# Optimization experiments

Hardware: AMD Instinct MI355X
Metric: run time of the kernel (lower is better)

The kernel has to match this reference:

```python
import jax, jax.numpy as jnp
import numpy as np

B, S, D_MODEL, D_K = 4, 4096, 1024, 64


def setup_inputs() -> dict:
    key = jax.random.key(0)
    kx, kq, kk, kv = jax.random.split(key, 4)
    x = jax.random.normal(kx, (B, S, D_MODEL), dtype=jnp.float32)
    # Linear(in, out) stores weight as (out, in); y = x @ W^T, no bias
    Wq = jax.random.normal(kq, (D_K, D_MODEL), dtype=jnp.float32) * (D_MODEL ** -0.5)
    Wk = jax.random.normal(kk, (D_K, D_MODEL), dtype=jnp.float32) * (D_MODEL ** -0.5)
    Wv = jax.random.normal(kv, (D_MODEL, D_MODEL), dtype=jnp.float32) * (D_MODEL ** -0.5)
    return {"x": x, "Wq": Wq, "Wk": Wk, "Wv": Wv}


def reference(x, Wq, Wk, Wv):
    # single-head scaled dot-product attention
    q = jnp.einsum('bsd,kd->bsk', x, Wq)   # [B,S,d_k]
    k = jnp.einsum('bsd,kd->bsk', x, Wk)   # [B,S,d_k]
    v = jnp.einsum('bsd,md->bsm', x, Wv)   # [B,S,d_model]
    scale = 1.0 / jnp.sqrt(jnp.asarray(q.shape[-1], q.dtype))
    scores = jnp.einsum('bqk,bsk->bqs', q, k) * scale  # [B,S,S]
    probs = jax.nn.softmax(scores, axis=-1)
    return jnp.einsum('bqs,bsm->bqm', probs, v)        # [B,S,d_model]
```

## Files before the change

kernel.cpp:

```cpp
#include <hip/hip_runtime.h>


#define DEV static __device__ __forceinline__

typedef __attribute__((ext_vector_type(8))) short bf16x8;
typedef __attribute__((ext_vector_type(4))) float f32x4;
typedef __attribute__((ext_vector_type(4))) unsigned short u16x4;
typedef __attribute__((ext_vector_type(8))) unsigned short u16x8;
typedef __attribute__((address_space(1))) void as1_void;
typedef __attribute__((address_space(3))) void as3_void;

DEV unsigned short f2bf(float f) {
  union { float f; unsigned u; } v; v.f = f;
  return (unsigned short)((v.u + 0x7FFFu + ((v.u >> 16) & 1u)) >> 16);
}

DEV unsigned pk_bf16(float a, float b) {
  union { float f; unsigned u; } va, vb;
  va.f = a; vb.f = b;
  return __builtin_amdgcn_perm(vb.u + 0x8000u, va.u + 0x8000u, 0x07060302u);
}

DEV void gload16(const void* g, void* l) {
  __builtin_amdgcn_global_load_lds((as1_void*)g, (as3_void*)l, 16, 0, 0);
}

DEV int swz(int row, int cb) { return (row << 7) + (cb ^ ((row & 7) << 4)); }

DEV void lgkm_barrier() {
  asm volatile("s_waitcnt lgkmcnt(0)" ::: "memory");
  __builtin_amdgcn_sched_barrier(0);
  __builtin_amdgcn_s_barrier();
  __builtin_amdgcn_sched_barrier(0);
}

__global__ __launch_bounds__(256) void cast_all_k(
    const float* __restrict__ x, const float* __restrict__ wq,
    const float* __restrict__ wk, const float* __restrict__ wv,
    unsigned short* __restrict__ xb, unsigned short* __restrict__ wcat, float sq) {
  const int stride = gridDim.x * blockDim.x;
  for (int i = blockIdx.x * blockDim.x + threadIdx.x; i < 2244608; i += stride) {
    const float* src; unsigned short* dst; float scale; int j;
    if (i < 2097152)      { src = x;  dst = xb;            scale = 1.f; j = i; }
    else if (i < 2105344) { src = wq; dst = wcat;          scale = sq;  j = i - 2097152; }
    else if (i < 2113536) { src = wk; dst = wcat + 65536;  scale = 1.f; j = i - 2105344; }
    else                  { src = wv; dst = wcat + 131072; scale = 1.f; j = i - 2113536; }
    const float4* p = (const float4*)src + (size_t)j * 2;
    float4 a = p[0], b = p[1];
    u16x8 r;
    r[0] = f2bf(a.x * scale); r[1] = f2bf(a.y * scale);
    r[2] = f2bf(a.z * scale); r[3] = f2bf(a.w * scale);
    r[4] = f2bf(b.x * scale); r[5] = f2bf(b.y * scale);
    r[6] = f2bf(b.z * scale); r[7] = f2bf(b.w * scale);
    *(u16x8*)(dst + (size_t)j * 8) = r;
  }
}

__global__ __launch_bounds__(256, 2) void gemm_qkv_k(
    const unsigned short* __restrict__ xb, const unsigned short* __restrict__ wcat,
    unsigned short* __restrict__ qk, unsigned short* __restrict__ vT) {
  __shared__ __align__(16) unsigned char smem[65536];
  unsigned char* sA = smem;
  unsigned char* sB = smem + 32768;
  const int tid = threadIdx.x;
  const int w = tid >> 6, lane = tid & 63, lo = lane & 15, hi = lane >> 4;
  const int wr = w >> 1, wc = w & 1;
  const int bn = blockIdx.x, m0 = blockIdx.y * 128, n0 = bn * 128;
  const char* aBase = (const char*)xb + (size_t)m0 * 2048;
  const char* bBase = (const char*)wcat + (size_t)n0 * 2048;

  const int soff = ((w * 4) << 10) + (lane << 4);
  f32x4 acc[4][4];
  const f32x4 z = {0.f, 0.f, 0.f, 0.f};
#pragma unroll
  for (int mi = 0; mi < 4; ++mi)
#pragma unroll
    for (int ni = 0; ni < 4; ++ni) acc[mi][ni] = z;

#pragma unroll
  for (int r2 = 0; r2 < 4; ++r2) {
    const int off = soff + (r2 << 10);
    const int row = off >> 7;
    const int cbs = (off & 127) ^ ((row & 7) << 4);
    gload16(aBase + (size_t)row * 2048 + cbs, sA + ((w * 4 + r2) << 10));
    gload16(bBase + (size_t)row * 2048 + cbs, sB + ((w * 4 + r2) << 10));
  }
  __syncthreads();

  int cur = 0;
  for (int k0 = 0; k0 < 1024; k0 += 64) {
    if (k0 + 64 < 1024) {
      const int nb = (cur ^ 1) * 16384;
#pragma unroll
      for (int r2 = 0; r2 < 4; ++r2) {
        const int off = soff + (r2 << 10);
        const int row = off >> 7;
        const int cbs = (off & 127) ^ ((row & 7) << 4);
        gload16(aBase + (size_t)row * 2048 + (k0 + 64) * 2 + cbs, sA + nb + ((w * 4 + r2) << 10));
        gload16(bBase + (size_t)row * 2048 + (k0 + 64) * 2 + cbs, sB + nb + ((w * 4 + r2) << 10));
      }
    }
    const int cb0 = cur * 16384;
#pragma unroll
    for (int kk = 0; kk < 2; ++kk) {
      const int cb = kk * 64 + hi * 16;
      bf16x8 af[4], bfv[4];
#pragma unroll
      for (int mi = 0; mi < 4; ++mi)
        af[mi] = *(const bf16x8*)(sA + cb0 + swz(wr * 64 + mi * 16 + lo, cb));
#pragma unroll
      for (int ni = 0; ni < 4; ++ni)
        bfv[ni] = *(const bf16x8*)(sB + cb0 + swz(wc * 64 + ni * 16 + lo, cb));
#pragma unroll
      for (int mi = 0; mi < 4; ++mi)
#pragma unroll
        for (int ni = 0; ni < 4; ++ni)
          acc[mi][ni] = __builtin_amdgcn_mfma_f32_16x16x32_bf16(af[mi], bfv[ni], acc[mi][ni], 0, 0, 0);
    }
    __syncthreads();
    cur ^= 1;
  }

  if (bn == 0) {
#pragma unroll
    for (int mi = 0; mi < 4; ++mi) {
      const int row = m0 + wr * 64 + mi * 16 + hi * 4;
#pragma unroll
      for (int ni = 0; ni < 4; ++ni) {
        const int col = wc * 64 + ni * 16 + lo;
#pragma unroll
        for (int r = 0; r < 4; ++r)
          qk[(size_t)(row + r) * 128 + col] = f2bf(acc[mi][ni][r]);
      }
    }
  } else {
#pragma unroll
    for (int mi = 0; mi < 4; ++mi) {
      const int grow = m0 + wr * 64 + mi * 16 + hi * 4;
      const int b = grow >> 12, s = grow & 4095;
#pragma unroll
      for (int ni = 0; ni < 4; ++ni) {
        const int vcol = (n0 - 128) + wc * 64 + ni * 16 + lo;
        u16x4 pk;
#pragma unroll
        for (int r = 0; r < 4; ++r) pk[r] = f2bf(acc[mi][ni][r]);
        *(u16x4*)(vT + (size_t)(b * 1024 + vcol) * 4096 + s) = pk;
      }
    }
  }
}

__global__ __launch_bounds__(512, 4) void pv_k(
    const unsigned short* __restrict__ qk, const unsigned short* __restrict__ vT,
    float* __restrict__ out) {
  __shared__ __align__(16) unsigned char smem[57344];
  unsigned char* sK = smem;
  unsigned char* sV = smem + 8192;
  unsigned char* sP = smem + 40960;
  const int tid = threadIdx.x;
  const int w = tid >> 6, lane = tid & 63, lo = lane & 15, hi = lane >> 4;
  const int wr = w >> 2, wc = w & 3;
  const int ck = blockIdx.x, qt = blockIdx.y, b = blockIdx.z;
  const char* qkB = (const char*)qk;
  const char* vTB = (const char*)vT;
  const size_t qrow0 = (size_t)(b * 4096 + qt * 128);
  const f32x4 z = {0.f, 0.f, 0.f, 0.f};

  const int q = w * 16 + lo;
  bf16x8 qf[2];
#pragma unroll
  for (int kk = 0; kk < 2; ++kk)
    qf[kk] = *(const bf16x8*)(qkB + (qrow0 + q) * 256 + kk * 64 + hi * 16);
  float lsum = 0.f;

  const int kc = w * 64 + lane;
  const int kRow = kc >> 3;
  const int kCbs = ((kc & 7) << 4) ^ ((kRow & 7) << 4);
  const char* kSrc = qkB + (size_t)(b * 4096 + kRow) * 256 + 128 + kCbs;

  const int g = lane & 3, dr = (lane >> 2) & 1, qq = lane >> 3;
  const int rr = (qq & 3) + ((qq >> 2) << 3) + (dr << 2);
  const int vRow0 = w * 16 + rr, vRow1 = vRow0 + 128;
  const char* vSrc0 = vTB + (size_t)(b * 1024 + ck * 256 + vRow0) * 8192 + g * 16;
  const char* vSrc1 = vTB + (size_t)(b * 1024 + ck * 256 + vRow1) * 8192 + g * 16;
  unsigned char* vDst0 = sV + vRow0 * 128;
  unsigned char* vDst1 = sV + vRow1 * 128;
  const int vX = g << 4, vR = (vRow0 & 7) << 4;

  const int qx7 = (q & 7) << 4;
  const int aP0 = (q << 7) + ((((hi >> 1) + 0) << 4) ^ qx7) + ((hi & 1) << 3);
  const int aP1 = (q << 7) + ((((hi >> 1) + 2) << 4) ^ qx7) + ((hi & 1) << 3);

  f32x4 acc[4][4];
#pragma unroll
  for (int mi = 0; mi < 4; ++mi)
#pragma unroll
    for (int ni = 0; ni < 4; ++ni) acc[mi][ni] = z;

  {
    float4 v0 = *(const float4*)(vSrc0);
    float4 v1 = *(const float4*)(vSrc1);
    if (w < 4) gload16(kSrc, sK + (w << 10));
    *(float4*)(vDst0 + (vX ^ vR)) = v0;
    *(float4*)(vDst1 + (vX ^ vR)) = v1;
  }
  __syncthreads();

  int cur = 0;
  for (int t = 0; t < 128; ++t) {
    float4 nv0, nv1;
    if (t < 127) {
      nv0 = *(const float4*)(vSrc0 + (size_t)(t + 1) * 64);
      nv1 = *(const float4*)(vSrc1 + (size_t)(t + 1) * 64);
      if (w < 4) gload16(kSrc + (size_t)(t + 1) * 8192, sK + (cur ^ 1) * 4096 + (w << 10));
    }
    f32x4 sv0 = z, sv1 = z;
#pragma unroll
    for (int kk = 0; kk < 2; ++kk) {
      bf16x8 kf0 = *(const bf16x8*)(sK + cur * 4096 + swz(lo, kk * 64 + hi * 16));
      bf16x8 kf1 = *(const bf16x8*)(sK + cur * 4096 + swz(16 + lo, kk * 64 + hi * 16));
      sv0 = __builtin_amdgcn_mfma_f32_16x16x32_bf16(kf0, qf[kk], sv0, 0, 0, 0);
      sv1 = __builtin_amdgcn_mfma_f32_16x16x32_bf16(kf1, qf[kk], sv1, 0, 0, 0);
    }
    {
      const float p0 = __builtin_amdgcn_exp2f(sv0[0]);
      const float p1 = __builtin_amdgcn_exp2f(sv0[1]);
      const float p2 = __builtin_amdgcn_exp2f(sv0[2]);
      const float p3 = __builtin_amdgcn_exp2f(sv0[3]);
      const float p4 = __builtin_amdgcn_exp2f(sv1[0]);
      const float p5 = __builtin_amdgcn_exp2f(sv1[1]);
      const float p6 = __builtin_amdgcn_exp2f(sv1[2]);
      const float p7 = __builtin_amdgcn_exp2f(sv1[3]);
      lsum += ((p0 + p1) + (p2 + p3)) + ((p4 + p5) + (p6 + p7));
      uint2 d0, d1;
      d0.x = pk_bf16(p0, p1); d0.y = pk_bf16(p2, p3);
      d1.x = pk_bf16(p4, p5); d1.y = pk_bf16(p6, p7);
      *(uint2*)(sP + aP0) = d0;
      *(uint2*)(sP + aP1) = d1;
    }
    lgkm_barrier();
    if (t < 127) {
      *(float4*)(vDst0 + ((((cur ^ 1) << 6) + vX) ^ vR)) = nv0;
      *(float4*)(vDst1 + ((((cur ^ 1) << 6) + vX) ^ vR)) = nv1;
    }
    __builtin_amdgcn_s_setprio(1);
    bf16x8 pa[4];
#pragma unroll
    for (int mi = 0; mi < 4; ++mi)
      pa[mi] = *(const bf16x8*)(sP + swz(wr * 64 + mi * 16 + lo, hi * 16));
#pragma unroll
    for (int ni = 0; ni < 4; ++ni) {
      bf16x8 vf = *(const bf16x8*)(sV + swz(wc * 64 + ni * 16 + lo, (cur << 6) + hi * 16));
#pragma unroll
      for (int mi = 0; mi < 4; ++mi)
        acc[mi][ni] = __builtin_amdgcn_mfma_f32_16x16x32_bf16(pa[mi], vf, acc[mi][ni], 0, 0, 0);
    }
    __builtin_amdgcn_s_setprio(0);
    __syncthreads();
    cur ^= 1;
  }

  lsum += __shfl_xor(lsum, 16, 64);
  lsum += __shfl_xor(lsum, 32, 64);
  float* lLds = (float*)smem;
  if (hi == 0) lLds[q] = lsum;
  __syncthreads();

#pragma unroll
  for (int mi = 0; mi < 4; ++mi)
#pragma unroll
    for (int r = 0; r < 4; ++r) {
      const int rloc = wr * 64 + mi * 16 + hi * 4 + r;
      const int grow = (int)qrow0 + rloc;
      const float linv = 1.0f / lLds[rloc];
#pragma unroll
      for (int ni = 0; ni < 4; ++ni) {
        const int col = ck * 256 + wc * 64 + ni * 16 + lo;
        out[(size_t)grow * 1024 + col] = acc[mi][ni][r] * linv;
      }
    }
}

extern "C" void kernel_launch(void* const* d_in, const int* in_sizes, int n_in,
                              void* d_out, int out_size, void* d_ws, size_t ws_size,
                              hipStream_t stream) {
  const float* x  = (const float*)d_in[0];
  const float* Wq = (const float*)d_in[1];
  const float* Wk = (const float*)d_in[2];
  const float* Wv = (const float*)d_in[3];

  char* ws = (char*)d_ws;
  unsigned short* xb    = (unsigned short*)(ws);
  unsigned short* wcat  = (unsigned short*)(ws + 33554432);
  unsigned short* qk    = (unsigned short*)(ws + 35913728);
  unsigned short* vT    = (unsigned short*)(ws + 40108032);

  const float SCALE_Q = 0.125f * 1.4426950408889634f;

  cast_all_k<<<2048, 256, 0, stream>>>(x, Wq, Wk, Wv, xb, wcat, SCALE_Q);
  gemm_qkv_k<<<dim3(9, 128), 256, 0, stream>>>(xb, wcat, qk, vT);
  pv_k<<<dim3(4, 32, 4), 512, 0, stream>>>(qk, vT, (float*)d_out);
}
```

Baseline: 249.3 us.

## Double the key tile per iteration and load V via direct global-to-LDS copies

The PV kernel now processes 64 keys per iteration instead of 32, halving loop trips and barriers. V tiles move from register-staged loads into single-buffered LDS loaded with global_load_lds, issued after the end-of-iteration barrier. K loads are also issued by all waves, and a vmcnt-based wait replaces the old lgkm-only barrier. LDS grows to 64KB, which may limit occupancy, and the single-buffered V load sits on the critical path after each barrier.

```diff
diff --git a/kernel.cpp b/kernel.cpp
--- a/kernel.cpp
+++ b/kernel.cpp
@@ -26,13 +26,6 @@
 }
 
 DEV int swz(int row, int cb) { return (row << 7) + (cb ^ ((row & 7) << 4)); }
-
-DEV void lgkm_barrier() {
-  asm volatile("s_waitcnt lgkmcnt(0)" ::: "memory");
-  __builtin_amdgcn_sched_barrier(0);
-  __builtin_amdgcn_s_barrier();
-  __builtin_amdgcn_sched_barrier(0);
-}
 
 __global__ __launch_bounds__(256) void cast_all_k(
     const float* __restrict__ x, const float* __restrict__ wq,
@@ -153,10 +146,10 @@
 __global__ __launch_bounds__(512, 4) void pv_k(
     const unsigned short* __restrict__ qk, const unsigned short* __restrict__ vT,
     float* __restrict__ out) {
-  __shared__ __align__(16) unsigned char smem[57344];
+  __shared__ __align__(16) unsigned char smem[65536];
   unsigned char* sK = smem;
-  unsigned char* sV = smem + 8192;
-  unsigned char* sP = smem + 40960;
+  unsigned char* sV = smem + 16384;
+  unsigned char* sP = smem + 49152;
   const int tid = threadIdx.x;
   const int w = tid >> 6, lane = tid & 63, lo = lane & 15, hi = lane >> 4;
   const int wr = w >> 2, wc = w & 3;
@@ -174,22 +167,23 @@
   float lsum = 0.f;
 
   const int kc = w * 64 + lane;
-  const int kRow = kc >> 3;
-  const int kCbs = ((kc & 7) << 4) ^ ((kRow & 7) << 4);
-  const char* kSrc = qkB + (size_t)(b * 4096 + kRow) * 256 + 128 + kCbs;
-
-  const int g = lane & 3, dr = (lane >> 2) & 1, qq = lane >> 3;
-  const int rr = (qq & 3) + ((qq >> 2) << 3) + (dr << 2);
-  const int vRow0 = w * 16 + rr, vRow1 = vRow0 + 128;
-  const char* vSrc0 = vTB + (size_t)(b * 1024 + ck * 256 + vRow0) * 8192 + g * 16;
-  const char* vSrc1 = vTB + (size_t)(b * 1024 + ck * 256 + vRow1) * 8192 + g * 16;
-  unsigned char* vDst0 = sV + vRow0 * 128;
-  unsigned char* vDst1 = sV + vRow1 * 128;
-  const int vX = g << 4, vR = (vRow0 & 7) << 4;
+  const int kRow = kc >> 3, kG = kc & 7;
+  const char* kSrc = qkB + (size_t)(b * 4096 + kRow) * 256 + 128 + ((kG ^ (kRow & 7)) << 4);
+  unsigned char* kDst = sK + (kc << 4);
+
+  const char* vSrcJ[4];
+#pragma unroll
+  for (int j = 0; j < 4; ++j) {
+    const int c = tid + j * 512;
+    const int row = c >> 3, g = c & 7;
+    vSrcJ[j] = vTB + (size_t)(b * 1024 + ck * 256 + row) * 8192 + ((g ^ (row & 7)) << 4);
+  }
 
   const int qx7 = (q & 7) << 4;
-  const int aP0 = (q << 7) + ((((hi >> 1) + 0) << 4) ^ qx7) + ((hi & 1) << 3);
-  const int aP1 = (q << 7) + ((((hi >> 1) + 2) << 4) ^ qx7) + ((hi & 1) << 3);
+  const int aP0 = (q << 7) + (((0 + (hi >> 1)) << 4) ^ qx7) + ((hi & 1) << 3);
+  const int aP1 = (q << 7) + (((2 + (hi >> 1)) << 4) ^ qx7) + ((hi & 1) << 3);
+  const int aP2 = (q << 7) + (((4 + (hi >> 1)) << 4) ^ qx7) + ((hi & 1) << 3);
+  const int aP3 = (q << 7) + (((6 + (hi >> 1)) << 4) ^ qx7) + ((hi & 1) << 3);
 
   f32x4 acc[4][4];
 #pragma unroll
@@ -197,66 +191,79 @@
 #pragma unroll
     for (int ni = 0; ni < 4; ++ni) acc[mi][ni] = z;
 
-  {
-    float4 v0 = *(const float4*)(vSrc0);
-    float4 v1 = *(const float4*)(vSrc1);
-    if (w < 4) gload16(kSrc, sK + (w << 10));
-    *(float4*)(vDst0 + (vX ^ vR)) = v0;
-    *(float4*)(vDst1 + (vX ^ vR)) = v1;
-  }
+#pragma unroll
+  for (int j = 0; j < 4; ++j) gload16(vSrcJ[j], sV + ((tid + j * 512) << 4));
+  gload16(kSrc, kDst);
   __syncthreads();
 
   int cur = 0;
-  for (int t = 0; t < 128; ++t) {
-    float4 nv0, nv1;
-    if (t < 127) {
-      nv0 = *(const float4*)(vSrc0 + (size_t)(t + 1) * 64);
-      nv1 = *(const float4*)(vSrc1 + (size_t)(t + 1) * 64);
-      if (w < 4) gload16(kSrc + (size_t)(t + 1) * 8192, sK + (cur ^ 1) * 4096 + (w << 10));
-    }
-    f32x4 sv0 = z, sv1 = z;
+  for (int t = 0; t < 64; ++t) {
+    gload16(kSrc + (size_t)((t + 1) & 63) * 16384, kDst + (cur ^ 1) * 8192);
+    f32x4 sv[4];
+    sv[0] = z; sv[1] = z; sv[2] = z; sv[3] = z;
 #pragma unroll
     for (int kk = 0; kk < 2; ++kk) {
-      bf16x8 kf0 = *(const bf16x8*)(sK + cur * 4096 + swz(lo, kk * 64 + hi * 16));
-      bf16x8 kf1 = *(const bf16x8*)(sK + cur * 4096 + swz(16 + lo, kk * 64 + hi * 16));
-      sv0 = __builtin_amdgcn_mfma_f32_16x16x32_bf16(kf0, qf[kk], sv0, 0, 0, 0);
-      sv1 = __builtin_amdgcn_mfma_f32_16x16x32_bf16(kf1, qf[kk], sv1, 0, 0, 0);
+#pragma unroll
+      for (int n = 0; n < 4; ++n) {
+        bf16x8 kf = *(const bf16x8*)(sK + cur * 8192 + swz(n * 16 + lo, kk * 64 + hi * 16));
+        sv[n] = __builtin_amdgcn_mfma_f32_16x16x32_bf16(kf, qf[kk], sv[n], 0, 0, 0);
+      }
     }
     {
-      const float p0 = __builtin_amdgcn_exp2f(sv0[0]);
-      const float p1 = __builtin_amdgcn_exp2f(sv0[1]);
-      const float p2 = __builtin_amdgcn_exp2f(sv0[2]);
-      const float p3 = __builtin_amdgcn_exp2f(sv0[3]);
-      const float p4 = __builtin_amdgcn_exp2f(sv1[0]);
-      const float p5 = __builtin_amdgcn_exp2f(sv1[1]);
-      const float p6 = __builtin_amdgcn_exp2f(sv1[2]);
-      const float p7 = __builtin_amdgcn_exp2f(sv1[3]);
-      lsum += ((p0 + p1) + (p2 + p3)) + ((p4 + p5) + (p6 + p7));
-      uint2 d0, d1;
-      d0.x = pk_bf16(p0, p1); d0.y = pk_bf16(p2, p3);
-      d1.x = pk_bf16(p4, p5); d1.y = pk_bf16(p6, p7);
+      const float p0 = __builtin_amdgcn_exp2f(sv[0][0]);
+      const float p1 = __builtin_amdgcn_exp2f(sv[0][1]);
+      const float p2 = __builtin_amdgcn_exp2f(sv[0][2]);
+      const float p3 = __builtin_amdgcn_exp2f(sv[0][3]);
+      const float p4 = __builtin_amdgcn_exp2f(sv[1][0]);
+      const float p5 = __builtin_amdgcn_exp2f(sv[1][1]);
+      const float p6 = __builtin_amdgcn_exp2f(sv[1][2]);
+      const float p7 = __builtin_amdgcn_exp2f(sv[1][3]);
+      const float p8 = __builtin_amdgcn_exp2f(sv[2][0]);
+      const float p9 = __builtin_amdgcn_exp2f(sv[2][1]);
+      const float pa_ = __builtin_amdgcn_exp2f(sv[2][2]);
+      const float pb_ = __builtin_amdgcn_exp2f(sv[2][3]);
+      const float pc_ = __builtin_amdgcn_exp2f(sv[3][0]);
+      const float pd_ = __builtin_amdgcn_exp2f(sv[3][1]);
+      const float pe_ = __builtin_amdgcn_exp2f(sv[3][2]);
+      const float pf_ = __builtin_amdgcn_exp2f(sv[3][3]);
+      lsum += (((p0 + p1) + (p2 + p3)) + ((p4 + p5) + (p6 + p7))) +
+              (((p8 + p9) + (pa_ + pb_)) + ((pc_ + pd_) + (pe_ + pf_)));
+      uint2 d0, d1, d2, d3;
+      d0.x = pk_bf16(p0, p1);  d0.y = pk_bf16(p2, p3);
+      d1.x = pk_bf16(p4, p5);  d1.y = pk_bf16(p6, p7);
+      d2.x = pk_bf16(p8, p9);  d2.y = pk_bf16(pa_, pb_);
+      d3.x = pk_bf16(pc_, pd_); d3.y = pk_bf16(pe_, pf_);
       *(uint2*)(sP + aP0) = d0;
       *(uint2*)(sP + aP1) = d1;
-    }
-    lgkm_barrier();
-    if (t < 127) {
-      *(float4*)(vDst0 + ((((cur ^ 1) << 6) + vX) ^ vR)) = nv0;
-      *(float4*)(vDst1 + ((((cur ^ 1) << 6) + vX) ^ vR)) = nv1;
-    }
+      *(uint2*)(sP + aP2) = d2;
+      *(uint2*)(sP + aP3) = d3;
+    }
+    asm volatile("s_waitcnt vmcnt(1) lgkmcnt(0)" ::: "memory");
+    __builtin_amdgcn_sched_barrier(0);
+    __builtin_amdgcn_s_barrier();
+    __builtin_amdgcn_sched_barrier(0);
     __builtin_amdgcn_s_setprio(1);
-    bf16x8 pa[4];
-#pragma unroll
-    for (int mi = 0; mi < 4; ++mi)
-      pa[mi] = *(const bf16x8*)(sP + swz(wr * 64 + mi * 16 + lo, hi * 16));
-#pragma unroll
-    for (int ni = 0; ni < 4; ++ni) {
-      bf16x8 vf = *(const bf16x8*)(sV + swz(wc * 64 + ni * 16 + lo, (cur << 6) + hi * 16));
+#pragma unroll
+    for (int kk = 0; kk < 2; ++kk) {
+      bf16x8 pa[4];
 #pragma unroll
       for (int mi = 0; mi < 4; ++mi)
-        acc[mi][ni] = __builtin_amdgcn_mfma_f32_16x16x32_bf16(pa[mi], vf, acc[mi][ni], 0, 0, 0);
+        pa[mi] = *(const bf16x8*)(sP + swz(wr * 64 + mi * 16 + lo, kk * 64 + hi * 16));
+#pragma unroll
+      for (int ni = 0; ni < 4; ++ni) {
+        bf16x8 vf = *(const bf16x8*)(sV + swz(wc * 64 + ni * 16 + lo, kk * 64 + hi * 16));
+#pragma unroll
+        for (int mi = 0; mi < 4; ++mi)
+          acc[mi][ni] = __builtin_amdgcn_mfma_f32_16x16x32_bf16(pa[mi], vf, acc[mi][ni], 0, 0, 0);
+      }
     }
     __builtin_amdgcn_s_setprio(0);
     __syncthreads();
+    if (t < 63) {
+#pragma unroll
+      for (int j = 0; j < 4; ++j)
+        gload16(vSrcJ[j] + (size_t)(t + 1) * 128, sV + ((tid + j * 512) << 4));
+    }
     cur ^= 1;
   }
 
```

Result: faster. 240.2 us (-3.6%).
